# Optimization experiments

Measured on AMD Instinct MI355X. Metric: run time of the kernel, lower is better.

The kernel has to match this reference:

```python
import jax, jax.numpy as jnp
import numpy as np

D = 1024          # feature dim (x_dim)
C = 32            # n classes (way)
SHOTS = 32
N_SUP = C * SHOTS
Q = 1024
REG = 0.5         # reg_param


def setup_inputs() -> dict:
    key = jax.random.key(0)
    ks = jax.random.split(key, 5)
    support_x = jax.random.normal(ks[0], (N_SUP, D), dtype=jnp.float32)
    query_x = jax.random.normal(ks[1], (Q, D), dtype=jnp.float32)
    labels_idx = (jnp.arange(N_SUP, dtype=jnp.int32) % C)  # every class present, equal shots
    m = jax.random.normal(ks[2], (1, D), dtype=jnp.float32) * 0.01
    kappa = jnp.float32(0.1)
    nu = jnp.float32(D)
    triu_diag = jnp.ones((D,), dtype=jnp.float32)
    triu_lower = jnp.eye(D, dtype=jnp.float32) + 0.01 * jax.random.normal(ks[3], (D, D), dtype=jnp.float32)
    return {"support_x": support_x, "query_x": query_x, "labels_idx": labels_idx,
            "m": m, "kappa": kappa, "nu": nu,
            "triu_diag": triu_diag, "triu_lower": triu_lower}


def _metaqda_fb(support_x, query_x, labels_idx, m, kappa, nu, triu_diag, triu_lower):
    onehot = jax.nn.one_hot(labels_idx, C, dtype=support_x.dtype)      # [N, C]
    Nj = jnp.sum(onehot, axis=0)                                       # [C]
    kappa_ = jnp.abs(kappa) + 1e-6
    nu_ = jnp.maximum(nu, jnp.float32(D - 1 + 1e-6))

    # Cholesky-factor prior scatter matrix: L @ L^T
    lower_mask = jnp.tril(jnp.ones((D, D), dtype=support_x.dtype), k=-1)
    L = jnp.diag(jnp.abs(triu_diag)) + triu_lower * lower_mask
    prior_S = L @ L.T                                                  # [D, D]

    # per-class sums (replaces python loop of rank-1 outer products with GEMMs)
    sum_x = onehot.T @ support_x                                       # [C, D]
    mean_x = sum_x / Nj[:, None]
    # sum_n x x^T per class: contract through [N,C,D] intermediate
    SXX = jnp.einsum('nc,nd,ne->cde', onehot, support_x, support_x)    # [C, D, D]

    kN = kappa_ + Nj                                                   # [C]
    mu = (kappa_ / kN)[:, None] * m + (Nj / kN)[:, None] * mean_x      # [C, D]

    mm = m.T @ m                                                       # [D, D]  (self_outer of [1,D])
    mumu = jnp.einsum('cd,ce->cde', mu, mu)                            # [C, D, D]
    S = prior_S[None] + SXX + kappa_ * mm[None] - kN[:, None, None] * mumu

    scale = (kN + 1.0) / ((nu_ + Nj - D + 1.0) * kN)                   # [C]
    sigma = S * scale[:, None, None]                                   # [C, D, D]

    sigma_inv = (1.0 - REG) * jnp.linalg.inv(sigma) + REG * jnp.eye(D, dtype=sigma.dtype)

    common = nu_ + Nj + 1.0 - D                                        # [C]
    _, logdet = jnp.linalg.slogdet(sigma)
    bias = (jax.lax.lgamma(0.5 * (common + D)) - jax.lax.lgamma(0.5 * common)
            - 0.5 * D * jnp.log(common) - 0.5 * logdet)                # [C]

    diff = query_x[:, None, :] - mu[None, :, :]                        # [Q, C, D]
    dist = jnp.einsum('qcd,cde,qce->qc', diff, sigma_inv, diff)        # [Q, C]
    preds = bias[None, :] - 0.5 * (common + D)[None, :] * jnp.log1p(dist / common[None, :])
    return preds


def reference(support_x, query_x, labels_idx, m, kappa, nu, triu_diag, triu_lower):
    return _metaqda_fb(support_x, query_x, labels_idx, m, kappa, nu, triu_diag, triu_lower)
```

## Files before the change

kernel.cpp:

```cpp
#include <hip/hip_runtime.h>
#include <math.h>

#define Dk 1024
#define Ck 32
#define Nk 1024
#define Qk 1024
#define REGP 0.5f
#define NB 64
#define NROWSV (Qk + Nk + Ck + 1)

#define CO_KAPPA 0
#define CO_NU    1
#define CO_NJ    2
#define CO_KN    34
#define CO_SCALE 66
#define CO_COMMON 98
#define CO_COEF  130
#define CO_BIASA 162
#define CO_BIASF 200

#define O_P    0u
#define O_W    2162688u
#define O_T    3211264u
#define O_MU   3473408u
#define O_QM   3506176u
#define O_MB   3538944u
#define O_MI   3578112u
#define O_QNY  3617280u
#define O_QNO  3618304u
#define O_MUN  3619328u
#define O_GMM  3619360u
#define O_EX   3619392u
#define O_CONS 3619408u
#define O_CIDX 3619664u
#define O_YH   3652432u
#define O_YM   4733776u
#define O_YL   5815120u
#define O_WH   6896464u
#define O_WM   7420752u
#define O_WL   7945040u
#define O_OH   8469328u
#define O_OM   9550672u
#define O_OL   10632016u

#define WS_DECL \
    float* P     = Wbuf + O_P;    (void)P; \
    float* W     = Wbuf + O_W;    (void)W; \
    float* Tb    = Wbuf + O_T;    (void)Tb; \
    float* QM    = Wbuf + O_QM;   (void)QM; \
    float* Mbuf  = Wbuf + O_MB;   (void)Mbuf; \
    float* Minv  = Wbuf + O_MI;   (void)Minv; \
    float* qny   = Wbuf + O_QNY;  (void)qny; \
    float* qno   = Wbuf + O_QNO;  (void)qno; \
    float* mun2o = Wbuf + O_MUN;  (void)mun2o; \
    float* gmm   = Wbuf + O_GMM;  (void)gmm; \
    float* extraf= Wbuf + O_EX;   (void)extraf; \
    float* cons  = Wbuf + O_CONS; (void)cons; \
    int*   cidx  = (int*)(Wbuf + O_CIDX); (void)cidx; \
    ushort* sYh = (ushort*)(Wbuf + O_YH); (void)sYh; \
    ushort* sYm = (ushort*)(Wbuf + O_YM); (void)sYm; \
    ushort* sYl = (ushort*)(Wbuf + O_YL); (void)sYl; \
    ushort* sWh = (ushort*)(Wbuf + O_WH); (void)sWh; \
    ushort* sWm = (ushort*)(Wbuf + O_WM); (void)sWm; \
    ushort* sWl = (ushort*)(Wbuf + O_WL); (void)sWl; \
    ushort* sOh = (ushort*)(Wbuf + O_OH); (void)sOh; \
    ushort* sOm = (ushort*)(Wbuf + O_OM); (void)sOm; \
    ushort* sOl = (ushort*)(Wbuf + O_OL); (void)sOl;

typedef __attribute__((ext_vector_type(8))) __bf16 bf16x8;
typedef __attribute__((ext_vector_type(4))) float f32x4;

#define MFMA(a, b, c) __builtin_amdgcn_mfma_f32_16x16x32_bf16(a, b, c, 0, 0, 0)

__device__ __forceinline__ ushort f2bf(float x) {
    unsigned u = __float_as_uint(x);
    return (ushort)((u + 0x7FFFu + ((u >> 16) & 1u)) >> 16);
}
__device__ __forceinline__ float bf2f(ushort h) {
    return __uint_as_float(((unsigned)h) << 16);
}
__device__ __forceinline__ void split1(float x, ushort& h, ushort& m, ushort& l) {
    h = f2bf(x);
    float r1 = x - bf2f(h);
    m = f2bf(r1);
    l = f2bf(r1 - bf2f(m));
}
__device__ __forceinline__ void split_store4(ushort* ph, ushort* pm, ushort* pl,
                                             size_t o, float4 v) {
    float vv[4] = {v.x, v.y, v.z, v.w};
    ushort4 H, M, L;
    ushort* Hp = (ushort*)&H; ushort* Mp = (ushort*)&M; ushort* Lp = (ushort*)&L;
#pragma unroll
    for (int c = 0; c < 4; ++c) split1(vv[c], Hp[c], Mp[c], Lp[c]);
    *(ushort4*)(ph + o) = H;
    *(ushort4*)(pm + o) = M;
    *(ushort4*)(pl + o) = L;
}

__device__ __forceinline__ float wave_red(float s) {
#pragma unroll
    for (int o = 32; o > 0; o >>= 1) s += __shfl_down(s, o, 64);
    return s;
}

#define LDSA(c, r, k8) ((c) * 5120 + (r) * 40 + (k8))
#define LDSB(c, r, k8) (15360 + (c) * 5120 + (r) * 40 + (k8))
#define LDS_HW 30720

__device__ __forceinline__ void tile_fetch2(
    bf16x8* ra, bf16x8* rb,
    const ushort* Ah, const ushort* Am, const ushort* Al, int aRow0, int aRowMax,
    const ushort* Bh, const ushort* Bm, const ushort* Bl, int bRow0,
    int kcol, int t)
{
    bf16x8 z = {};
#pragma unroll
    for (int u = 0; u < 6; ++u) {
        int comp = u >> 1;
        int idx = ((u & 1) << 8) + t;
        int row = idx >> 2, kg = idx & 3;
        const ushort* As = (comp == 0) ? Ah : ((comp == 1) ? Am : Al);
        int gr = aRow0 + row;
        ra[u] = (gr < aRowMax) ? *(const bf16x8*)(As + (size_t)gr * 1024 + kcol + kg * 8) : z;
        const ushort* Bs = (comp == 0) ? Bh : ((comp == 1) ? Bm : Bl);
        rb[u] = *(const bf16x8*)(Bs + (size_t)(bRow0 + row) * 1024 + kcol + kg * 8);
    }
}

__device__ __forceinline__ void tile_store2(ushort* lds, const bf16x8* ra, const bf16x8* rb, int t) {
#pragma unroll
    for (int u = 0; u < 6; ++u) {
        int comp = u >> 1;
        int idx = ((u & 1) << 8) + t;
        int row = idx >> 2, kg = idx & 3;
        *(bf16x8*)(lds + LDSA(comp, row, kg * 8)) = ra[u];
        *(bf16x8*)(lds + LDSB(comp, row, kg * 8)) = rb[u];
    }
}

__device__ __forceinline__ void tile_compute2(const ushort* lds, f32x4 acc[2][8],
                                              int w, int lr, int lk) {
    bf16x8 af[2][3];
#pragma unroll
    for (int rf = 0; rf < 2; ++rf)
#pragma unroll
        for (int c = 0; c < 3; ++c)
            af[rf][c] = *(const bf16x8*)(lds + LDSA(c, w * 32 + rf * 16 + lr, lk * 8));
#pragma unroll
    for (int cf = 0; cf < 8; ++cf) {
        bf16x8 bh = *(const bf16x8*)(lds + LDSB(0, cf * 16 + lr, lk * 8));
        bf16x8 bm = *(const bf16x8*)(lds + LDSB(1, cf * 16 + lr, lk * 8));
        bf16x8 bl = *(const bf16x8*)(lds + LDSB(2, cf * 16 + lr, lk * 8));
#pragma unroll
        for (int rf = 0; rf < 2; ++rf) {
            f32x4 a = acc[rf][cf];
            a = MFMA(af[rf][0], bh, a);
            a = MFMA(af[rf][0], bm, a);
            a = MFMA(af[rf][1], bh, a);
            a = MFMA(af[rf][0], bl, a);
            a = MFMA(af[rf][2], bh, a);
            a = MFMA(af[rf][1], bm, a);
            acc[rf][cf] = a;
        }
    }
}

__device__ __forceinline__ void tile_gemm2(
    ushort* lds, f32x4 acc[2][8],
    const ushort* Ah, const ushort* Am, const ushort* Al, int aRow0, int aRowMax,
    const ushort* Bh, const ushort* Bm, const ushort* Bl, int bRow0,
    int kbase, int ksteps, int t)
{
    const int w = t >> 6, lr = t & 15, lk = (t >> 4) & 3;
    bf16x8 ra[6], rb[6];
    tile_fetch2(ra, rb, Ah, Am, Al, aRow0, aRowMax, Bh, Bm, Bl, bRow0, kbase * 32, t);
    tile_store2(lds, ra, rb, t);
    __syncthreads();
    for (int kt = 0; kt < ksteps; ++kt) {
        if (kt + 1 < ksteps)
            tile_fetch2(ra, rb, Ah, Am, Al, aRow0, aRowMax, Bh, Bm, Bl, bRow0,
                        (kbase + kt + 1) * 32, t);
        tile_compute2(lds, acc, w, lr, lk);
        __syncthreads();
        if (kt + 1 < ksteps)
            tile_store2(lds, ra, rb, t);
        __syncthreads();
    }
}

__device__ __forceinline__ void fetch4(float4* reg, const float* src, int ld,
                                       int rowbase, int rowmax, int colbase, int t) {
#pragma unroll
    for (int u = 0; u < 4; ++u) {
        int slot = t + u * 256;
        int r = slot >> 4, c4 = slot & 15;
        int gr = rowbase + r;
        reg[u] = (gr < rowmax) ? *(const float4*)(src + (size_t)gr * ld + colbase + c4 * 4)
                               : make_float4(0.f, 0.f, 0.f, 0.f);
    }
}
__device__ __forceinline__ void stT(float* dst, const float4* reg, int t) {
#pragma unroll
    for (int u = 0; u < 4; ++u) {
        int slot = t + u * 256;
        int r = slot >> 4, c4 = slot & 15;
        dst[(c4 * 4 + 0) * 68 + r] = reg[u].x;
        dst[(c4 * 4 + 1) * 68 + r] = reg[u].y;
        dst[(c4 * 4 + 2) * 68 + r] = reg[u].z;
        dst[(c4 * 4 + 3) * 68 + r] = reg[u].w;
    }
}
__device__ __forceinline__ void stN(float* dst, const float4* reg, int t) {
#pragma unroll
    for (int u = 0; u < 4; ++u) {
        int slot = t + u * 256;
        int r = slot >> 4, c4 = slot & 15;
        *(float4*)(dst + r * 68 + c4 * 4) = reg[u];
    }
}
__device__ __forceinline__ void gemm16(const float* At, const float* Bt,
                                       float acc[4][4], int tx, int ty) {
#pragma unroll 4
    for (int kk = 0; kk < NB; ++kk) {
        float4 a = *(const float4*)(At + kk * 68 + ty * 4);
        float4 b = *(const float4*)(Bt + kk * 68 + tx * 4);
        float av[4] = {a.x, a.y, a.z, a.w};
        float bv[4] = {b.x, b.y, b.z, b.w};
#pragma unroll
        for (int r = 0; r < 4; ++r)
#pragma unroll
            for (int s = 0; s < 4; ++s) acc[r][s] += av[r] * bv[s];
    }
}
__device__ __forceinline__ void mm_task(
    const float* aSrc, int aLd, int aRow, int aRowMax, int aCol, int aRowStep, int aColStep,
    const float* bSrc, int bLd, int bRow, int bRowMax, int bCol, int bRowStep, int bColStep,
    bool bTrans, int k0, int k1,
    float acc[4][4], float* smA, float* smB, int t, int tx, int ty)
{
    float4 ra[4], rb[4];
    fetch4(ra, aSrc, aLd, aRow + k0 * aRowStep, aRowMax, aCol + k0 * aColStep, t);
    fetch4(rb, bSrc, bLd, bRow + k0 * bRowStep, bRowMax, bCol + k0 * bColStep, t);
    stT(smA, ra, t);
    if (bTrans) stT(smB, rb, t); else stN(smB, rb, t);
    __syncthreads();
    for (int kt = k0; kt < k1; ++kt) {
        if (kt + 1 < k1) {
            fetch4(ra, aSrc, aLd, aRow + (kt + 1) * aRowStep, aRowMax, aCol + (kt + 1) * aColStep, t);
            fetch4(rb, bSrc, bLd, bRow + (kt + 1) * bRowStep, bRowMax, bCol + (kt + 1) * bColStep, t);
        }
        gemm16(smA, smB, acc, tx, ty);
        __syncthreads();
        if (kt + 1 < k1) {
            stT(smA, ra, t);
            if (bTrans) stT(smB, rb, t); else stN(smB, rb, t);
        }
        __syncthreads();
    }
}

__global__ __launch_bounds__(256) void k_p0(const float* qx, const int* labels,
                                            const float* mvec, const float* kappa,
                                            const float* nu, const float* td,
                                            const float* tl, float* Wbuf) {
    __shared__ __align__(16) float smem[9216];
    float* smA = smem;
    float* sX  = smem + 8704;
    WS_DECL
    float* Yo32 = Wbuf;
    const int t = threadIdx.x;
    const int lane = t & 63, wv = t >> 6;
    const int tau = blockIdx.x;

    if (tau == 0) {
        int* scnt = (int*)sX;
        if (t < Ck) scnt[t] = 0;
        __syncthreads();
        for (int n = t; n < Nk; n += 256) {
            int l = labels[n];
            int pos = atomicAdd(&scnt[l], 1);
            cidx[l * Nk + pos] = n;
        }
        __syncthreads();
        if (t < Ck) {
            float kap = fabsf(kappa[0]) + 1e-6f;
            float nu_ = fmaxf(nu[0], (float)(Dk - 1) + 1e-6f);
            float Njf = (float)scnt[t];
            float kN = kap + Njf;
            if (t == 0) { cons[CO_KAPPA] = kap; cons[CO_NU] = nu_; }
            cons[CO_NJ + t] = Njf;
            cons[CO_KN + t] = kN;
            cons[CO_SCALE + t] = (kN + 1.0f) / ((nu_ + Njf - (float)Dk + 1.0f) * kN);
            float common = nu_ + Njf + 1.0f - (float)Dk;
            cons[CO_COMMON + t] = common;
            cons[CO_COEF + t] = 0.5f * (common + (float)Dk);
            cons[CO_BIASA + t] = lgammaf(0.5f * (common + (float)Dk)) - lgammaf(0.5f * common)
                                 - 0.5f * (float)Dk * logf(common);
        }
    } else if (tau == 1) {
        float s = 0.f;
        for (int i = t; i < Dk; i += 256) s += logf(fabsf(td[i]));
        s = wave_red(s);
        if (lane == 0) sX[wv] = s;
        __syncthreads();
        if (t == 0) extraf[0] = 2.f * (sX[0] + sX[1] + sX[2] + sX[3]);
    } else if (tau < 18) {
        int b0 = (tau - 2) * NB;
        for (int idx = t; idx < 64 * 64; idx += 256) {
            int m = idx >> 6, i = idx & 63;
            smem[i * 72 + m] = (m > i) ? tl[(size_t)(b0 + m) * Dk + b0 + i] : 0.f;
        }
        if (t < 64) smem[4608 + t] = 1.f / fabsf(td[b0 + t]);
        __syncthreads();
        if (t < 64) {
            const int j = t;
            float r[64];
#pragma unroll
            for (int m = 0; m < 64; ++m) r[m] = (m == j) ? 1.f : 0.f;
#pragma unroll
            for (int i = 0; i < 64; ++i) {
                float x = r[i] * smem[4608 + i];
                r[i] = x;
#pragma unroll
                for (int g = (i >> 2); g < 16; ++g) {
                    float4 lt = *(const float4*)&smem[i * 72 + g * 4];
                    r[g * 4 + 0] -= lt.x * x;
                    r[g * 4 + 1] -= lt.y * x;
                    r[g * 4 + 2] -= lt.z * x;
                    r[g * 4 + 3] -= lt.w * x;
                }
            }
#pragma unroll
            for (int i = 0; i < 64; ++i)
                W[(size_t)(b0 + i) * Dk + b0 + j] = r[i];
        }
    } else if (tau < 21) {
        int base = (tau - 18) * 13056;
        for (int i = t; i < 13056 && base + i < 39168; i += 256) Mbuf[base + i] = 0.f;
    } else if (tau == 21) {
        if (t < 32) { mun2o[t] = 0.f; gmm[t] = 0.f; }
        for (int i = t; i < 8192; i += 256)
            ((float4*)QM)[i] = make_float4(0, 0, 0, 0);
    } else if (tau < 86) {
        int rbase = (tau - 22) * 16;
        for (int j = wv; j < 16; j += 4) {
            const float* row = qx + (size_t)(rbase + j) * Dk;
            float s = 0.f;
            for (int d = lane; d < Dk; d += 64) { float v = row[d]; s += v * v; }
            s = wave_red(s);
            if (lane == 0) qno[rbase + j] = s;
        }
    } else if (tau < 150) {
        int rbase = (tau - 86) * 16;
        for (int j = 0; j < 16; ++j) {
            int r = rbase + j;
            float4 v = ((const float4*)(qx + (size_t)r * Dk))[t];
            split_store4(sYh, sYm, sYl, (size_t)r * 1024 + (size_t)t * 4, v);
        }
    } else if (tau == 150) {
        float4 v = ((const float4*)mvec)[t];
        split_store4(sYh, sYm, sYl, (size_t)2080 * 1024 + (size_t)t * 4, v);
    } else {
        int rbase = (tau - 151) * 16;
        for (int j = 0; j < 16; ++j)
            ((float4*)(Yo32 + (size_t)(rbase + j) * 1024))[t] = make_float4(0, 0, 0, 0);
    }
}

__global__ __launch_bounds__(256) void k_p1(const float* sx, const float* mvec, float* Wbuf) {
    __shared__ float sX[512];
    WS_DECL
    const int t = threadIdx.x;
    const int lane = t & 63, wv = t >> 6;
    const int tau = blockIdx.x;
    if (tau < 128) {
        int c = tau >> 2;
        int d = ((tau & 3) << 8) + t;
        int Nj = (int)cons[CO_NJ + c];
        float kap = cons[CO_KAPPA], kN = cons[CO_KN + c];
        float acc = 0.f;
        for (int s = 0; s < Nj; ++s) acc += sx[(size_t)cidx[c * Nk + s] * Dk + d];
        float muv = (kap * mvec[d] + acc) / kN;
        size_t o = (size_t)(2048 + c) * 1024 + d;
        ushort h, m_, l_;
        split1(muv, h, m_, l_);
        sYh[o] = h; sYm[o] = m_; sYl[o] = l_;
        float s2 = wave_red(muv * muv);
        if (lane == 0) sX[wv] = s2;
        __syncthreads();
        if (t == 0) atomicAdd(&mun2o[c], sX[0] + sX[1] + sX[2] + sX[3]);
    } else {
        int rbase = (tau - 128) * 16;
        for (int j = 0; j < 16; ++j) {
            int n = rbase + j;
            int srcrow = cidx[(n >> 5) * Nk + (n & 31)];
            float4 v = ((const float4*)(sx + (size_t)srcrow * Dk))[t];
            split_store4(sYh, sYm, sYl, (size_t)(1024 + n) * 1024 + (size_t)t * 4, v);
        }
    }
}

__global__ __launch_bounds__(256) void k_t1(const float* tl, float* Wbuf) {
    __shared__ __align__(16) float smem[8704];
    float* smA = smem;
    float* smB = smem + 4352;
    WS_DECL
    const int t = threadIdx.x;
    const int tx = t & 15, ty = t >> 4;
    const int BIG = 1 << 30;
    int pb = blockIdx.x * 128;
    float acc[4][4] = {};
    mm_task(tl, Dk, pb + 64, BIG, pb, 0, NB,
            W, Dk, pb, BIG, pb, NB, 0, false, 0, 1,
            acc, smA, smB, t, tx, ty);
    {
        float4 ra[4];
        fetch4(ra, W, Dk, pb + 64, BIG, pb + 64, t);
#pragma unroll
        for (int r = 0; r < 4; ++r)
#pragma unroll
            for (int s = 0; s < 4; ++s)
                smB[(ty * 4 + r) * 68 + tx * 4 + s] = acc[r][s];
        stT(smA, ra, t);
    }
    __syncthreads();
    float acc2[4][4] = {};
    gemm16(smA, smB, acc2, tx, ty);
    __syncthreads();
#pragma unroll
    for (int r = 0; r < 4; ++r)
#pragma unroll
        for (int s = 0; s < 4; ++s)
            W[(size_t)(pb + 64 + ty * 4 + r) * Dk + pb + tx * 4 + s] = -acc2[r][s];
}

__global__ __launch_bounds__(256) void k_tr_a(const float* tl, float* Wbuf, int h, int ht) {
    __shared__ __align__(16) float smem[8704];
    float* smA = smem;
    float* smB = smem + 4352;
    WS_DECL
    const int t = threadIdx.x;
    const int tx = t & 15, ty = t >> 4;
    const int BIG = 1 << 30;
    int tau = blockIdx.x;
    int p = tau / (ht * ht), rr = tau % (ht * ht);
    int i = rr / ht, j = rr % ht;
    int pb = p * 2 * h;
    float acc[4][4] = {};
    mm_task(tl, Dk, pb + h + i * NB, BIG, pb, 0, NB,
            W, Dk, pb, BIG, pb + j * NB, NB, 0, false, 0, ht,
            acc, smA, smB, t, tx, ty);
    float* Tp = Tb + (size_t)p * h * h;
#pragma unroll
    for (int r = 0; r < 4; ++r)
#pragma unroll
        for (int s = 0; s < 4; ++s)
            Tp[(size_t)(i * NB + ty * 4 + r) * h + j * NB + tx * 4 + s] = acc[r][s];
}

__global__ __launch_bounds__(256) void k_tr_b(float* Wbuf, int h, int ht) {
    __shared__ __align__(16) float smem[8704];
    float* smA = smem;
    float* smB = smem + 4352;
    WS_DECL
    const int t = threadIdx.x;
    const int tx = t & 15, ty = t >> 4;
    const int BIG = 1 << 30;
    int tau = blockIdx.x;
    int p = tau / (ht * ht), rr = tau % (ht * ht);
    int i = rr / ht, j = rr % ht;
    int pb = p * 2 * h;
    const float* Tp = Tb + (size_t)p * h * h;
    float acc[4][4] = {};
    mm_task(W, Dk, pb + h + i * NB, BIG, pb + h, 0, NB,
            Tp, h, 0, BIG, j * NB, NB, 0, false, 0, ht,
            acc, smA, smB, t, tx, ty);
#pragma unroll
    for (int r = 0; r < 4; ++r)
#pragma unroll
        for (int s = 0; s < 4; ++s)
            W[(size_t)(pb + h + i * NB + ty * 4 + r) * Dk + pb + j * NB + tx * 4 + s] = -acc[r][s];
}

__global__ __launch_bounds__(256) void k_cvtw(float* Wbuf) {
    WS_DECL
    const int t = threadIdx.x;
#pragma unroll
    for (int u = 0; u < 4; ++u) {
        unsigned g = blockIdx.x * 1024u + u * 256u + t;
        int row = g >> 8, col4 = (g & 255) * 4;
        float4 v = ((const float4*)W)[g];
        if (col4 + 0 > row) v.x = 0.f;
        if (col4 + 1 > row) v.y = 0.f;
        if (col4 + 2 > row) v.z = 0.f;
        if (col4 + 3 > row) v.w = 0.f;
        split_store4(sWh, sWm, sWl, (size_t)g * 4, v);
    }
}

__global__ __launch_bounds__(256) void k_yg(float* Wbuf) {
    __shared__ __align__(16) ushort lds[LDS_HW];
    WS_DECL
    float* Yo32 = Wbuf;
    const int t = threadIdx.x;
    int e = blockIdx.x;
    int q = e / 17, rt = e % 17;
    int jt2, kc;
    if (q < 4)       { jt2 = 7; kc = q; }
    else if (q < 8)  { jt2 = 6; kc = q - 4; }
    else if (q < 11) { jt2 = 5; kc = q - 8; }
    else if (q < 14) { jt2 = 4; kc = q - 11; }
    else if (q < 16) { jt2 = 3; kc = q - 14; }
    else if (q < 18) { jt2 = 2; kc = q - 16; }
    else if (q == 18){ jt2 = 1; kc = 0; }
    else             { jt2 = 0; kc = 0; }
    int ksteps = min(8, 4 * (jt2 + 1) - kc * 8);
    f32x4 acc[2][8] = {};
    tile_gemm2(lds, acc, sYh, sYm, sYl, rt * 128, 2081,
               sWh, sWm, sWl, jt2 * 128, kc * 8, ksteps, t);
    const int w = t >> 6, lr = t & 15, lk = (t >> 4) & 3;
#pragma unroll
    for (int rf = 0; rf < 2; ++rf)
#pragma unroll
        for (int cf = 0; cf < 8; ++cf)
#pragma unroll
            for (int r = 0; r < 4; ++r) {
                int grow = rt * 128 + w * 32 + rf * 16 + lk * 4 + r;
                if (grow < NROWSV)
                    atomicAdd(&Yo32[(size_t)grow * 1024 + jt2 * 128 + cf * 16 + lr],
                              acc[rf][cf][r]);
            }
}

__global__ __launch_bounds__(256) void k_cvto(float* Wbuf) {
    WS_DECL
    float* Yo32 = Wbuf;
    const int t = threadIdx.x;
    int rbase = blockIdx.x * 4;
#pragma unroll
    for (int j = 0; j < 4; ++j) {
        int r = rbase + j;
        float4 v = ((const float4*)(Yo32 + (size_t)r * 1024))[t];
        split_store4(sOh, sOm, sOl, (size_t)r * 1024 + (size_t)t * 4, v);
    }
    if (rbase < 1088) {
#pragma unroll
        for (int j = 0; j < 4; ++j)
            ((float4*)(Yo32 + (size_t)(rbase + j) * 1024))[t] = make_float4(0, 0, 0, 0);
    }
}

__global__ __launch_bounds__(256) void k_p4m(float* Wbuf) {
    __shared__ __align__(16) ushort lds[LDS_HW];
    WS_DECL
    const int t = threadIdx.x;
    int e = blockIdx.x;
    const int w = t >> 6, lr = t & 15, lk = (t >> 4) & 3;
    f32x4 acc[2][8] = {};
    if (e < 288) {
        int tile = e >> 2, kc = e & 3;
        int mt = tile >> 3, qt2 = tile & 7;
        tile_gemm2(lds, acc, sOh, sOm, sOl, 1024 + mt * 128, 2081,
                   sOh, sOm, sOl, qt2 * 128, kc * 8, 8, t);
#pragma unroll
        for (int rf = 0; rf < 2; ++rf)
#pragma unroll
            for (int cf = 0; cf < 8; ++cf)
#pragma unroll
                for (int r = 0; r < 4; ++r) {
                    int n = mt * 128 + w * 32 + rf * 16 + lk * 4 + r;
                    if (n < Nk + Ck + 1)
                        atomicAdd(&P[(size_t)n * 1024 + qt2 * 128 + cf * 16 + lr],
                                  acc[rf][cf][r]);
                }
    } else {
        int f = e - 288;
        int qt2 = f >> 2, kc = f & 3;
        tile_gemm2(lds, acc, sYh, sYm, sYl, 2048, 2080,
                   sYh, sYm, sYl, qt2 * 128, kc * 8, 8, t);
#pragma unroll
        for (int rf = 0; rf < 2; ++rf)
#pragma unroll
            for (int cf = 0; cf < 8; ++cf)
#pragma unroll
                for (int r = 0; r < 4; ++r) {
                    int rq = w * 32 + rf * 16 + lk * 4 + r;
                    if (rq < 32)
                        atomicAdd(&QM[(size_t)rq * 1024 + qt2 * 128 + cf * 16 + lr],
                                  acc[rf][cf][r]);
                }
    }
}

__global__ __launch_bounds__(256) void k_gram(float* Wbuf) {
    __shared__ __align__(16) float smA[34 * 68];
    WS_DECL
    const int t = threadIdx.x;
    const int lane = t & 63, wv = t >> 6;
    const int tau = blockIdx.x;
    if (tau < 128) {
        int c = tau >> 2, kc = tau & 3;
        float accg[5];
        int iu[5], ju[5];
#pragma unroll
        for (int u = 0; u < 5; ++u) {
            int e = t + u * 256;
            iu[u] = e / 34; ju[u] = e - iu[u] * 34;
            accg[u] = 0.f;
        }
        for (int kt = kc * 4; kt < kc * 4 + 4; ++kt) {
            for (int e2 = t; e2 < 34 * NB; e2 += 256) {
                int i = e2 >> 6, k = e2 & 63;
                int yr = (i < 32) ? (Qk + c * 32 + i) : ((i == 32) ? (Qk + Nk + c) : (Qk + Nk + Ck));
                size_t o = (size_t)yr * 1024 + kt * NB + k;
                smA[i * 68 + k] = bf2f(sOh[o]) + bf2f(sOm[o]) + bf2f(sOl[o]);
            }
            __syncthreads();
#pragma unroll
            for (int u = 0; u < 5; ++u) {
                int e = t + u * 256;
                if (e < 1156) {
                    float s = 0.f;
                    for (int k = 0; k < NB; ++k) s += smA[iu[u] * 68 + k] * smA[ju[u] * 68 + k];
                    accg[u] += s;
                }
            }
            __syncthreads();
        }
#pragma unroll
        for (int u = 0; u < 5; ++u) {
            int e = t + u * 256;
            if (e < 1156)
                atomicAdd(&Mbuf[c * 1224 + iu[u] * 36 + ju[u]], accg[u]);
        }
    } else {
        int rbase = (tau - 128) * 16;
        for (int j = wv; j < 16; j += 4) {
            size_t ro = (size_t)(rbase + j) * 1024;
            float s = 0.f;
            for (int d = lane; d < Dk; d += 64) {
                size_t o = ro + d;
                float v = bf2f(sOh[o]) + bf2f(sOm[o]) + bf2f(sOl[o]);
                s += v * v;
            }
            s = wave_red(s);
            if (lane == 0) qny[rbase + j] = s;
        }
    }
}

__global__ __launch_bounds__(64) void k_p5(float* Wbuf) {
    __shared__ __align__(16) float A[34 * 36];
    WS_DECL
    const int t = threadIdx.x;
    const int c = blockIdx.x;
    float kN = cons[CO_KN + c], kap = cons[CO_KAPPA];
    for (int e = t; e < 34 * 34; e += 64) {
        int i = e / 34, j = e - i * 34;
        A[i * 36 + j] = Mbuf[c * 1224 + i * 36 + j];
    }
    __syncthreads();
    if (t == 0) {
        gmm[c] = A[32 * 36 + 32];
        A[32 * 36 + 32] += -1.f / kN;
        A[33 * 36 + 33] += 1.f / kap;
    }
    if (t < 32) A[t * 36 + t] += 1.f;
    __syncthreads();
    float ldacc = 0.f;
    for (int j = 0; j < 34; ++j) {
        float piv = A[j * 36 + j];
        float pinv = 1.f / piv;
        if (t == 0) ldacc += logf(fabsf(piv));
        if (t < 34 && t != j) A[j * 36 + t] *= pinv;
        __syncthreads();
        if (t < 34) {
            if (t != j) {
                float f = A[t * 36 + j];
                float4* rowT = (float4*)(A + t * 36);
                const float4* rowJ = (const float4*)(A + j * 36);
#pragma unroll
                for (int k4 = 0; k4 < 8; ++k4) {
                    float4 rv = rowT[k4], pv = rowJ[k4];
                    rv.x -= f * pv.x; rv.y -= f * pv.y;
                    rv.z -= f * pv.z; rv.w -= f * pv.w;
                    rowT[k4] = rv;
                }
                A[t * 36 + 32] -= f * A[j * 36 + 32];
                A[t * 36 + 33] -= f * A[j * 36 + 33];
                A[t * 36 + j] = -f * pinv;
            } else {
                A[j * 36 + j] = pinv;
            }
        }
        __syncthreads();
    }
    for (int e = t; e < 34 * 34; e += 64) {
        int i = e / 34, j = e - i * 34;
        Minv[c * 1224 + i * 36 + j] = A[i * 36 + j];
    }
    if (t == 0) {
        float scale = cons[CO_SCALE + c];
        float logdet = (float)Dk * logf(scale) + extraf[0] + logf(kN) + logf(kap) + ldacc;
        cons[CO_BIASF + c] = cons[CO_BIASA + c] - 0.5f * logdet;
    }
}

__global__ __launch_bounds__(256) void k_p6(float* Wbuf, float* out) {
    __shared__ __align__(16) float smem[3904];
    float* Mi  = smem;
    float* wL  = smem + 1200;
    float* gsm = smem + 3520;
    float* red = smem + 3520 + 128;
    WS_DECL
    const int t = threadIdx.x;
    const int tau = blockIdx.x;
    int qt = tau >> 5, c = tau & 31;
    for (int e = t; e < 34 * 34; e += 256) {
        int i = e / 34, j = e - i * 34;
        Mi[i * 35 + j] = Minv[c * 1224 + i * 36 + j];
    }
    if (t < 34)
        gsm[t] = (t < 32) ? Mbuf[c * 1224 + t * 36 + 32]
                          : ((t == 32) ? gmm[c] : Mbuf[c * 1224 + 33 * 36 + 32]);
    __syncthreads();
    for (int e = t; e < 34 * NB; e += 256) {
        int i = e >> 6, qq = e & 63;
        int prow = (i < 32) ? (c * 32 + i) : ((i == 32) ? (Nk + c) : (Nk + Ck));
        wL[i * 68 + qq] = P[(size_t)prow * Qk + qt * NB + qq] - gsm[i];
    }
    __syncthreads();
    {
        int q = t & 63, part = t >> 6;
        int start = (part < 2) ? part * 9 : 18 + (part - 2) * 8;
        int cnt = (part < 2) ? 9 : 8;
        float partial = 0.f;
        for (int i = start; i < start + cnt; ++i) {
            float v = 0.f;
            for (int j = 0; j < 34; ++j) v += Mi[i * 35 + j] * wL[j * 68 + q];
            partial += v * wL[i * 68 + q];
        }
        red[part * 64 + q] = partial;
    }
    __syncthreads();
    if (t < 64) {
        int q = t;
        float quad = red[q] + red[64 + q] + red[128 + q] + red[192 + q];
        int qg = qt * NB + q;
        float w32 = wL[32 * 68 + q];
        float ydist2 = qny[qg] - 2.f * w32 - gmm[c];
        float dd = qno[qg] + mun2o[c] - 2.f * QM[(size_t)c * Qk + qg];
        float scale = cons[CO_SCALE + c], common = cons[CO_COMMON + c];
        float dist = (1.f - REGP) / scale * (ydist2 - quad) + REGP * dd;
        out[(size_t)qg * Ck + c] = cons[CO_BIASF + c] - cons[CO_COEF + c] * log1pf(dist / common);
    }
}

extern "C" void kernel_launch(void* const* d_in, const int* in_sizes, int n_in,
                              void* d_out, int out_size, void* d_ws, size_t ws_size,
                              hipStream_t stream) {
    const float* sx = (const float*)d_in[0];
    const float* qx = (const float*)d_in[1];
    const int* labels = (const int*)d_in[2];
    const float* mvec = (const float*)d_in[3];
    const float* kappa = (const float*)d_in[4];
    const float* nu = (const float*)d_in[5];
    const float* td = (const float*)d_in[6];
    const float* tl = (const float*)d_in[7];
    float* W = (float*)d_ws;
    float* out = (float*)d_out;

    hipLaunchKernelGGL(k_p0, dim3(283), dim3(256), 0, stream,
                       qx, labels, mvec, kappa, nu, td, tl, W);
    hipLaunchKernelGGL(k_p1, dim3(192), dim3(256), 0, stream, sx, mvec, W);
    hipLaunchKernelGGL(k_t1, dim3(8), dim3(256), 0, stream, tl, W);
    for (int l = 2; l <= 4; ++l) {
        int h = 32 << l, ht = h >> 6, pairs = 16 >> l;
        int nt = pairs * ht * ht;
        hipLaunchKernelGGL(k_tr_a, dim3(nt), dim3(256), 0, stream, tl, W, h, ht);
        hipLaunchKernelGGL(k_tr_b, dim3(nt), dim3(256), 0, stream, W, h, ht);
    }
    hipLaunchKernelGGL(k_cvtw, dim3(256), dim3(256), 0, stream, W);
    hipLaunchKernelGGL(k_yg, dim3(340), dim3(256), 0, stream, W);
    hipLaunchKernelGGL(k_cvto, dim3(528), dim3(256), 0, stream, W);
    hipLaunchKernelGGL(k_p4m, dim3(320), dim3(256), 0, stream, W);
    hipLaunchKernelGGL(k_gram, dim3(192), dim3(256), 0, stream, W);
    hipLaunchKernelGGL(k_p5, dim3(32), dim3(64), 0, stream, W);
    hipLaunchKernelGGL(k_p6, dim3(512), dim3(256), 0, stream, W, out);
}
```

Before: 349.7 us.

## Load GEMM A fragments directly to registers and fuse k_t1 into k_p1

The split-bf16 MFMA GEMM now keeps only the B tile in LDS and loads A fragments straight from global memory into registers, double-buffered across k-steps. Each wave now owns a 64x64 output sub-tile instead of 32x128, which halves LDS use and changes the per-wave fragment reuse. The small k_t1 triangular-inverse kernel is folded into extra blocks of k_p1 to save one launch. The risks are more register pressure, uncoalesced direct global loads for A, and fewer B reads per A fragment.

```diff
diff --git a/kernel.cpp b/kernel.cpp
--- a/kernel.cpp
+++ b/kernel.cpp
@@ -103,56 +103,56 @@
     return s;
 }
 
-#define LDSA(c, r, k8) ((c) * 5120 + (r) * 40 + (k8))
-#define LDSB(c, r, k8) (15360 + (c) * 5120 + (r) * 40 + (k8))
-#define LDS_HW 30720
-
-__device__ __forceinline__ void tile_fetch2(
-    bf16x8* ra, bf16x8* rb,
-    const ushort* Ah, const ushort* Am, const ushort* Al, int aRow0, int aRowMax,
-    const ushort* Bh, const ushort* Bm, const ushort* Bl, int bRow0,
-    int kcol, int t)
-{
-    bf16x8 z = {};
+#define LDSB3(c, r, k8) ((c) * 5120 + (r) * 40 + (k8))
+#define LDS_HW3 15360
+
+__device__ __forceinline__ void b_fetch3(bf16x8* rb,
+                                         const ushort* Bh, const ushort* Bm, const ushort* Bl,
+                                         int bRow0, int kcol, int t) {
 #pragma unroll
     for (int u = 0; u < 6; ++u) {
         int comp = u >> 1;
         int idx = ((u & 1) << 8) + t;
         int row = idx >> 2, kg = idx & 3;
-        const ushort* As = (comp == 0) ? Ah : ((comp == 1) ? Am : Al);
-        int gr = aRow0 + row;
-        ra[u] = (gr < aRowMax) ? *(const bf16x8*)(As + (size_t)gr * 1024 + kcol + kg * 8) : z;
         const ushort* Bs = (comp == 0) ? Bh : ((comp == 1) ? Bm : Bl);
         rb[u] = *(const bf16x8*)(Bs + (size_t)(bRow0 + row) * 1024 + kcol + kg * 8);
     }
 }
-
-__device__ __forceinline__ void tile_store2(ushort* lds, const bf16x8* ra, const bf16x8* rb, int t) {
+__device__ __forceinline__ void b_store3(ushort* lds, const bf16x8* rb, int t) {
 #pragma unroll
     for (int u = 0; u < 6; ++u) {
         int comp = u >> 1;
         int idx = ((u & 1) << 8) + t;
         int row = idx >> 2, kg = idx & 3;
-        *(bf16x8*)(lds + LDSA(comp, row, kg * 8)) = ra[u];
-        *(bf16x8*)(lds + LDSB(comp, row, kg * 8)) = rb[u];
-    }
-}
-
-__device__ __forceinline__ void tile_compute2(const ushort* lds, f32x4 acc[2][8],
-                                              int w, int lr, int lk) {
-    bf16x8 af[2][3];
-#pragma unroll
-    for (int rf = 0; rf < 2; ++rf)
-#pragma unroll
-        for (int c = 0; c < 3; ++c)
-            af[rf][c] = *(const bf16x8*)(lds + LDSA(c, w * 32 + rf * 16 + lr, lk * 8));
-#pragma unroll
-    for (int cf = 0; cf < 8; ++cf) {
-        bf16x8 bh = *(const bf16x8*)(lds + LDSB(0, cf * 16 + lr, lk * 8));
-        bf16x8 bm = *(const bf16x8*)(lds + LDSB(1, cf * 16 + lr, lk * 8));
-        bf16x8 bl = *(const bf16x8*)(lds + LDSB(2, cf * 16 + lr, lk * 8));
-#pragma unroll
-        for (int rf = 0; rf < 2; ++rf) {
+        *(bf16x8*)(lds + LDSB3(comp, row, kg * 8)) = rb[u];
+    }
+}
+__device__ __forceinline__ void a_fetch3(bf16x8 af[4][3],
+                                         const ushort* Ah, const ushort* Am, const ushort* Al,
+                                         int arowT, int aRowMax, int kcol, int lk) {
+    bf16x8 z = {};
+#pragma unroll
+    for (int rf = 0; rf < 4; ++rf) {
+        int gr = arowT + rf * 16;
+        bool ok = gr < aRowMax;
+#pragma unroll
+        for (int c = 0; c < 3; ++c) {
+            const ushort* As = (c == 0) ? Ah : ((c == 1) ? Am : Al);
+            af[rf][c] = ok ? *(const bf16x8*)(As + (size_t)gr * 1024 + kcol + lk * 8) : z;
+        }
+    }
+}
+
+__device__ __forceinline__ void tile_compute3(const ushort* lds, f32x4 acc[4][4],
+                                              bf16x8 af[4][3], int bcol0, int lr, int lk) {
+#pragma unroll
+    for (int cf = 0; cf < 4; ++cf) {
+        int brow = bcol0 + cf * 16 + lr;
+        bf16x8 bh = *(const bf16x8*)(lds + LDSB3(0, brow, lk * 8));
+        bf16x8 bm = *(const bf16x8*)(lds + LDSB3(1, brow, lk * 8));
+        bf16x8 bl = *(const bf16x8*)(lds + LDSB3(2, brow, lk * 8));
+#pragma unroll
+        for (int rf = 0; rf < 4; ++rf) {
             f32x4 a = acc[rf][cf];
             a = MFMA(af[rf][0], bh, a);
             a = MFMA(af[rf][0], bm, a);
@@ -165,25 +165,34 @@
     }
 }
 
-__device__ __forceinline__ void tile_gemm2(
-    ushort* lds, f32x4 acc[2][8],
+__device__ __forceinline__ void tile_gemm3(
+    ushort* lds, f32x4 acc[4][4],
     const ushort* Ah, const ushort* Am, const ushort* Al, int aRow0, int aRowMax,
     const ushort* Bh, const ushort* Bm, const ushort* Bl, int bRow0,
     int kbase, int ksteps, int t)
 {
     const int w = t >> 6, lr = t & 15, lk = (t >> 4) & 3;
-    bf16x8 ra[6], rb[6];
-    tile_fetch2(ra, rb, Ah, Am, Al, aRow0, aRowMax, Bh, Bm, Bl, bRow0, kbase * 32, t);
-    tile_store2(lds, ra, rb, t);
+    const int arowT = aRow0 + (w >> 1) * 64 + lr;
+    const int bcol0 = (w & 1) * 64;
+    bf16x8 rb[6], afc[4][3], afn[4][3];
+    b_fetch3(rb, Bh, Bm, Bl, bRow0, kbase * 32, t);
+    a_fetch3(afc, Ah, Am, Al, arowT, aRowMax, kbase * 32, lk);
+    b_store3(lds, rb, t);
     __syncthreads();
     for (int kt = 0; kt < ksteps; ++kt) {
-        if (kt + 1 < ksteps)
-            tile_fetch2(ra, rb, Ah, Am, Al, aRow0, aRowMax, Bh, Bm, Bl, bRow0,
-                        (kbase + kt + 1) * 32, t);
-        tile_compute2(lds, acc, w, lr, lk);
-        __syncthreads();
-        if (kt + 1 < ksteps)
-            tile_store2(lds, ra, rb, t);
+        if (kt + 1 < ksteps) {
+            b_fetch3(rb, Bh, Bm, Bl, bRow0, (kbase + kt + 1) * 32, t);
+            a_fetch3(afn, Ah, Am, Al, arowT, aRowMax, (kbase + kt + 1) * 32, lk);
+        }
+        tile_compute3(lds, acc, afc, bcol0, lr, lk);
+        __syncthreads();
+        if (kt + 1 < ksteps) {
+            b_store3(lds, rb, t);
+#pragma unroll
+            for (int rf = 0; rf < 4; ++rf)
+#pragma unroll
+                for (int c = 0; c < 3; ++c) afc[rf][c] = afn[rf][c];
+        }
         __syncthreads();
     }
 }
@@ -264,7 +273,6 @@
                                             const float* nu, const float* td,
                                             const float* tl, float* Wbuf) {
     __shared__ __align__(16) float smem[9216];
-    float* smA = smem;
     float* sX  = smem + 8704;
     WS_DECL
     float* Yo32 = Wbuf;
@@ -367,13 +375,15 @@
     }
 }
 
-__global__ __launch_bounds__(256) void k_p1(const float* sx, const float* mvec, float* Wbuf) {
-    __shared__ float sX[512];
+__global__ __launch_bounds__(256) void k_p1(const float* sx, const float* mvec,
+                                            const float* tl, float* Wbuf) {
+    __shared__ __align__(16) float smem[8704];
     WS_DECL
     const int t = threadIdx.x;
     const int lane = t & 63, wv = t >> 6;
     const int tau = blockIdx.x;
     if (tau < 128) {
+        float* sX = smem;
         int c = tau >> 2;
         int d = ((tau & 3) << 8) + t;
         int Nj = (int)cons[CO_NJ + c];
@@ -389,7 +399,7 @@
         if (lane == 0) sX[wv] = s2;
         __syncthreads();
         if (t == 0) atomicAdd(&mun2o[c], sX[0] + sX[1] + sX[2] + sX[3]);
-    } else {
+    } else if (tau < 192) {
         int rbase = (tau - 128) * 16;
         for (int j = 0; j < 16; ++j) {
             int n = rbase + j;
@@ -397,41 +407,36 @@
             float4 v = ((const float4*)(sx + (size_t)srcrow * Dk))[t];
             split_store4(sYh, sYm, sYl, (size_t)(1024 + n) * 1024 + (size_t)t * 4, v);
         }
-    }
-}
-
-__global__ __launch_bounds__(256) void k_t1(const float* tl, float* Wbuf) {
-    __shared__ __align__(16) float smem[8704];
-    float* smA = smem;
-    float* smB = smem + 4352;
-    WS_DECL
-    const int t = threadIdx.x;
-    const int tx = t & 15, ty = t >> 4;
-    const int BIG = 1 << 30;
-    int pb = blockIdx.x * 128;
-    float acc[4][4] = {};
-    mm_task(tl, Dk, pb + 64, BIG, pb, 0, NB,
-            W, Dk, pb, BIG, pb, NB, 0, false, 0, 1,
-            acc, smA, smB, t, tx, ty);
-    {
-        float4 ra[4];
-        fetch4(ra, W, Dk, pb + 64, BIG, pb + 64, t);
+    } else {
+        float* smA = smem;
+        float* smB = smem + 4352;
+        const int tx = t & 15, ty = t >> 4;
+        const int BIG = 1 << 30;
+        int pb = (tau - 192) * 128;
+        float acc[4][4] = {};
+        mm_task(tl, Dk, pb + 64, BIG, pb, 0, NB,
+                W, Dk, pb, BIG, pb, NB, 0, false, 0, 1,
+                acc, smA, smB, t, tx, ty);
+        {
+            float4 ra[4];
+            fetch4(ra, W, Dk, pb + 64, BIG, pb + 64, t);
+#pragma unroll
+            for (int r = 0; r < 4; ++r)
+#pragma unroll
+                for (int s = 0; s < 4; ++s)
+                    smB[(ty * 4 + r) * 68 + tx * 4 + s] = acc[r][s];
+            stT(smA, ra, t);
+        }
+        __syncthreads();
+        float acc2[4][4] = {};
+        gemm16(smA, smB, acc2, tx, ty);
+        __syncthreads();
 #pragma unroll
         for (int r = 0; r < 4; ++r)
 #pragma unroll
             for (int s = 0; s < 4; ++s)
-                smB[(ty * 4 + r) * 68 + tx * 4 + s] = acc[r][s];
-        stT(smA, ra, t);
-    }
-    __syncthreads();
-    float acc2[4][4] = {};
-    gemm16(smA, smB, acc2, tx, ty);
-    __syncthreads();
-#pragma unroll
-    for (int r = 0; r < 4; ++r)
-#pragma unroll
-        for (int s = 0; s < 4; ++s)
-            W[(size_t)(pb + 64 + ty * 4 + r) * Dk + pb + tx * 4 + s] = -acc2[r][s];
+                W[(size_t)(pb + 64 + ty * 4 + r) * Dk + pb + tx * 4 + s] = -acc2[r][s];
+    }
 }
 
 __global__ __launch_bounds__(256) void k_tr_a(const float* tl, float* Wbuf, int h, int ht) {
@@ -499,7 +504,7 @@
 }
 
 __global__ __launch_bounds__(256) void k_yg(float* Wbuf) {
-    __shared__ __align__(16) ushort lds[LDS_HW];
+    __shared__ __align__(16) ushort lds[LDS_HW3];
     WS_DECL
     float* Yo32 = Wbuf;
     const int t = threadIdx.x;
@@ -515,19 +520,19 @@
     else if (q == 18){ jt2 = 1; kc = 0; }
     else             { jt2 = 0; kc = 0; }
     int ksteps = min(8, 4 * (jt2 + 1) - kc * 8);
-    f32x4 acc[2][8] = {};
-    tile_gemm2(lds, acc, sYh, sYm, sYl, rt * 128, 2081,
+    f32x4 acc[4][4] = {};
+    tile_gemm3(lds, acc, sYh, sYm, sYl, rt * 128, 2081,
                sWh, sWm, sWl, jt2 * 128, kc * 8, ksteps, t);
     const int w = t >> 6, lr = t & 15, lk = (t >> 4) & 3;
 #pragma unroll
-    for (int rf = 0; rf < 2; ++rf)
-#pragma unroll
-        for (int cf = 0; cf < 8; ++cf)
+    for (int rf = 0; rf < 4; ++rf)
+#pragma unroll
+        for (int cf = 0; cf < 4; ++cf)
 #pragma unroll
             for (int r = 0; r < 4; ++r) {
-                int grow = rt * 128 + w * 32 + rf * 16 + lk * 4 + r;
+                int grow = rt * 128 + (w >> 1) * 64 + rf * 16 + lk * 4 + r;
                 if (grow < NROWSV)
-                    atomicAdd(&Yo32[(size_t)grow * 1024 + jt2 * 128 + cf * 16 + lr],
+                    atomicAdd(&Yo32[(size_t)grow * 1024 + jt2 * 128 + (w & 1) * 64 + cf * 16 + lr],
                               acc[rf][cf][r]);
             }
 }
@@ -551,42 +556,42 @@
 }
 
 __global__ __launch_bounds__(256) void k_p4m(float* Wbuf) {
-    __shared__ __align__(16) ushort lds[LDS_HW];
+    __shared__ __align__(16) ushort lds[LDS_HW3];
     WS_DECL
     const int t = threadIdx.x;
     int e = blockIdx.x;
     const int w = t >> 6, lr = t & 15, lk = (t >> 4) & 3;
-    f32x4 acc[2][8] = {};
+    f32x4 acc[4][4] = {};
     if (e < 288) {
         int tile = e >> 2, kc = e & 3;
         int mt = tile >> 3, qt2 = tile & 7;
-        tile_gemm2(lds, acc, sOh, sOm, sOl, 1024 + mt * 128, 2081,
+        tile_gemm3(lds, acc, sOh, sOm, sOl, 1024 + mt * 128, 2081,
                    sOh, sOm, sOl, qt2 * 128, kc * 8, 8, t);
 #pragma unroll
-        for (int rf = 0; rf < 2; ++rf)
-#pragma unroll
-            for (int cf = 0; cf < 8; ++cf)
+        for (int rf = 0; rf < 4; ++rf)
+#pragma unroll
+            for (int cf = 0; cf < 4; ++cf)
 #pragma unroll
                 for (int r = 0; r < 4; ++r) {
-                    int n = mt * 128 + w * 32 + rf * 16 + lk * 4 + r;
+                    int n = mt * 128 + (w >> 1) * 64 + rf * 16 + lk * 4 + r;
                     if (n < Nk + Ck + 1)
-                        atomicAdd(&P[(size_t)n * 1024 + qt2 * 128 + cf * 16 + lr],
+                        atomicAdd(&P[(size_t)n * 1024 + qt2 * 128 + (w & 1) * 64 + cf * 16 + lr],
                                   acc[rf][cf][r]);
                 }
     } else {
         int f = e - 288;
         int qt2 = f >> 2, kc = f & 3;
-        tile_gemm2(lds, acc, sYh, sYm, sYl, 2048, 2080,
+        tile_gemm3(lds, acc, sYh, sYm, sYl, 2048, 2080,
                    sYh, sYm, sYl, qt2 * 128, kc * 8, 8, t);
 #pragma unroll
-        for (int rf = 0; rf < 2; ++rf)
-#pragma unroll
-            for (int cf = 0; cf < 8; ++cf)
+        for (int rf = 0; rf < 4; ++rf)
+#pragma unroll
+            for (int cf = 0; cf < 4; ++cf)
 #pragma unroll
                 for (int r = 0; r < 4; ++r) {
-                    int rq = w * 32 + rf * 16 + lk * 4 + r;
+                    int rq = (w >> 1) * 64 + rf * 16 + lk * 4 + r;
                     if (rq < 32)
-                        atomicAdd(&QM[(size_t)rq * 1024 + qt2 * 128 + cf * 16 + lr],
+                        atomicAdd(&QM[(size_t)rq * 1024 + qt2 * 128 + (w & 1) * 64 + cf * 16 + lr],
                                   acc[rf][cf][r]);
                 }
     }
@@ -772,8 +777,7 @@
 
     hipLaunchKernelGGL(k_p0, dim3(283), dim3(256), 0, stream,
                        qx, labels, mvec, kappa, nu, td, tl, W);
-    hipLaunchKernelGGL(k_p1, dim3(192), dim3(256), 0, stream, sx, mvec, W);
-    hipLaunchKernelGGL(k_t1, dim3(8), dim3(256), 0, stream, tl, W);
+    hipLaunchKernelGGL(k_p1, dim3(200), dim3(256), 0, stream, sx, mvec, tl, W);
     for (int l = 2; l <= 4; ++l) {
         int h = 32 << l, ht = h >> 6, pairs = 16 >> l;
         int nt = pairs * ht * ht;
```

Result: no change. 348.8 us (-0.3%).
